# Optimization experiments

Hardware: AMD Instinct MI355X
Metric: run time of the kernel (lower is better)

Reference implementation:

```python
import jax, jax.numpy as jnp
import numpy as np

D_MODEL = 2048
N_HEADS = 16
D_K = D_MODEL // N_HEADS  # 128


def setup_inputs() -> dict:
    key = jax.random.key(0)
    ks = jax.random.split(key, 12)
    B, S = 2, 2048
    std = 1.0 / np.sqrt(D_MODEL)
    inp = {
        "query": jax.random.normal(ks[0], (B, S, D_MODEL), jnp.float32),
        "key": jax.random.normal(ks[1], (B, S, D_MODEL), jnp.float32),
        "value": jax.random.normal(ks[2], (B, S, D_MODEL), jnp.float32),
        "w_q": jax.random.normal(ks[3], (D_MODEL, D_MODEL), jnp.float32) * std,
        "b_q": jnp.zeros((D_MODEL,), jnp.float32),
        "w_k": jax.random.normal(ks[4], (D_MODEL, D_MODEL), jnp.float32) * std,
        "b_k": jnp.zeros((D_MODEL,), jnp.float32),
        "w_v": jax.random.normal(ks[5], (D_MODEL, D_MODEL), jnp.float32) * std,
        "b_v": jnp.zeros((D_MODEL,), jnp.float32),
        "w_o": jax.random.normal(ks[6], (D_MODEL, D_MODEL), jnp.float32) * std,
        "b_o": jnp.zeros((D_MODEL,), jnp.float32),
        # fractional scale numerator / denominator per head; ratio ~ 1/sqrt(d_k)
        "scale_alpha": jnp.full((N_HEADS,), 1.0, jnp.float32),
        "scale_beta": jnp.full((N_HEADS,), float(np.sqrt(D_K)), jnp.float32),
    }
    return inp


def reference(query, key, value, w_q, b_q, w_k, b_k, w_v, b_v, w_o, b_o,
              scale_alpha, scale_beta):
    B, S, _ = query.shape
    # projections (torch Linear: x @ W^T + b)
    Q = (query @ w_q.T + b_q).reshape(B, S, N_HEADS, D_K).transpose(0, 2, 1, 3)
    K = (key @ w_k.T + b_k).reshape(B, S, N_HEADS, D_K).transpose(0, 2, 1, 3)
    V = (value @ w_v.T + b_v).reshape(B, S, N_HEADS, D_K).transpose(0, 2, 1, 3)
    # per-head fractional scale alpha/beta (computed under no_grad in torch)
    scales = jax.lax.stop_gradient(scale_alpha / jnp.maximum(scale_beta, 1.0))
    scores = jnp.einsum("bhqd,bhkd->bhqk", Q, K) * scales[None, :, None, None]
    attn = jax.nn.softmax(scores, axis=-1)  # dropout is identity in eval
    out = jnp.einsum("bhqk,bhkd->bhqd", attn, V)
    out = out.transpose(0, 2, 1, 3).reshape(B, S, D_MODEL)
    return out @ w_o.T + b_o
```

## Files before the change

### kernel.cpp

```cpp
#include <hip/hip_runtime.h>
#include <cstdint>

#define S_LEN   2048
#define DMODEL  2048
#define NHEADS  16
#define DK      128
#define MROWS   4096

typedef _Float16 f16;
using f16x8 = __attribute__((ext_vector_type(8))) _Float16;
using f16x4 = __attribute__((ext_vector_type(4))) _Float16;
using f32x4 = __attribute__((ext_vector_type(4))) float;

typedef const __attribute__((address_space(1))) unsigned int gu32;
typedef __attribute__((address_space(3))) unsigned int lu32;

__device__ __forceinline__ void gl2lds16(const void* g, void* l) {
    __builtin_amdgcn_global_load_lds((gu32*)g, (lu32*)l, 16, 0, 0);
}

__global__ __launch_bounds__(256) void cvt_all(
    const float* __restrict__ q, const float* __restrict__ k,
    const float* __restrict__ v, const float* __restrict__ wq,
    const float* __restrict__ wk, const float* __restrict__ wv,
    const float* __restrict__ wo,
    f16* cq, f16* ck, f16* cv, f16* cwq, f16* cwk, f16* cwv, f16* cwo)
{
    const int b = blockIdx.x;
    const float* src; f16* dst; int base;
    if      (b <  2048) { src = q;  dst = cq;  base = b; }
    else if (b <  4096) { src = k;  dst = ck;  base = b - 2048; }
    else if (b <  6144) { src = v;  dst = cv;  base = b - 4096; }
    else if (b <  7168) { src = wq; dst = cwq; base = b - 6144; }
    else if (b <  8192) { src = wk; dst = cwk; base = b - 7168; }
    else if (b <  9216) { src = wv; dst = cwv; base = b - 8192; }
    else                { src = wo; dst = cwo; base = b - 9216; }
    const int i = base * 1024 + threadIdx.x;
#pragma unroll
    for (int u = 0; u < 4; ++u) {
        float4 x = ((const float4*)src)[i + u * 256];
        f16x4 o; o[0] = (f16)x.x; o[1] = (f16)x.y; o[2] = (f16)x.z; o[3] = (f16)x.w;
        ((f16x4*)dst)[i + u * 256] = o;
    }
}

template<int MODE>
__device__ __forceinline__ void gemm_core(
    const f16* __restrict__ A, const f16* __restrict__ W,
    const float* __restrict__ bias, void* __restrict__ Cout,
    const float* __restrict__ sa, const float* __restrict__ sb,
    f16* __restrict__ As, f16* __restrict__ Bs)
{
    const int tid = threadIdx.x;
    const int bm = blockIdx.y * 128;
    const int bn = blockIdx.x * 128;
    const int wid = tid >> 6;
    const int ln = tid & 15;
    const int quad = (tid & 63) >> 4;
    const int wm = (wid >> 1) * 64;
    const int wn = (wid & 1) * 64;
    const int K = DMODEL, N = DMODEL;

    f32x4 acc[4][4];
#pragma unroll
    for (int i = 0; i < 4; ++i)
#pragma unroll
        for (int j = 0; j < 4; ++j)
            acc[i][j] = (f32x4){0.f, 0.f, 0.f, 0.f};

    const int srow = tid >> 3;
    const int schk = ((tid & 7) ^ ((tid >> 3) & 7)) * 8;
    const f16* ga = A + (size_t)(bm + srow) * K + schk;
    const f16* gb = W + (size_t)(bn + srow) * K + schk;

    for (int k0 = 0; k0 < K; k0 += 64) {
        __syncthreads();
#pragma unroll
        for (int u = 0; u < 4; ++u)
            gl2lds16(ga + k0 + (size_t)(u * 32) * K, As + u * 2048 + tid * 8);
#pragma unroll
        for (int u = 0; u < 4; ++u)
            gl2lds16(gb + k0 + (size_t)(u * 32) * K, Bs + u * 2048 + tid * 8);
        __syncthreads();

#pragma unroll
        for (int kq = 0; kq < 2; ++kq) {
            f16x8 af[4], bf[4];
            const int rc = ((kq * 4 + quad) ^ (ln & 7)) * 8;
#pragma unroll
            for (int i = 0; i < 4; ++i)
                af[i] = *(const f16x8*)&As[(wm + i * 16 + ln) * 64 + rc];
#pragma unroll
            for (int j = 0; j < 4; ++j)
                bf[j] = *(const f16x8*)&Bs[(wn + j * 16 + ln) * 64 + rc];
#pragma unroll
            for (int i = 0; i < 4; ++i)
#pragma unroll
                for (int j = 0; j < 4; ++j)
                    acc[i][j] = __builtin_amdgcn_mfma_f32_16x16x32_f16(
                        af[i], bf[j], acc[i][j], 0, 0, 0);
        }
    }

#pragma unroll
    for (int j = 0; j < 4; ++j) {
        const int n = bn + wn + j * 16 + ln;
        const float bn_ = bias[n];
        const int h = n >> 7;
        const int d = n & (DK - 1);
        float scq = 1.0f;
        if constexpr (MODE == 3) scq = sa[h] / fmaxf(sb[h], 1.0f);
#pragma unroll
        for (int i = 0; i < 4; ++i) {
            const int m0 = bm + wm + i * 16 + quad * 4;
            if constexpr (MODE == 0) {
#pragma unroll
                for (int reg = 0; reg < 4; ++reg)
                    ((float*)Cout)[(size_t)(m0 + reg) * N + n] =
                        acc[i][j][reg] + bn_;
            } else if constexpr (MODE == 2) {
                const int bb = m0 >> 11;
                const int ss = m0 & (S_LEN - 1);
                f16x4 o;
#pragma unroll
                for (int reg = 0; reg < 4; ++reg)
                    o[reg] = (f16)(acc[i][j][reg] + bn_);
                *(f16x4*)&((f16*)Cout)[
                    (((size_t)(bb * NHEADS + h) * DK + d) * S_LEN + ss)] = o;
            } else {
                const int bb = m0 >> 11;
                const int ss = m0 & (S_LEN - 1);
                f16* dst = (f16*)Cout +
                    (((size_t)(bb * NHEADS + h) * S_LEN + ss) * DK + d);
#pragma unroll
                for (int reg = 0; reg < 4; ++reg) {
                    float v = acc[i][j][reg] + bn_;
                    if constexpr (MODE == 3) v *= scq;
                    dst[reg * DK] = (f16)v;
                }
            }
        }
    }
}

__global__ __launch_bounds__(256) void qkv_gemm(
    const f16* Aq, const f16* Ak, const f16* Av,
    const f16* Wq, const f16* Wk, const f16* Wv,
    const float* bq, const float* bk, const float* bv,
    f16* Oq, f16* Ok, f16* Ov, const float* sa, const float* sb)
{
    __shared__ f16 As[128 * 64];
    __shared__ f16 Bs[128 * 64];
    const int z = blockIdx.z;
    if (z == 0)      gemm_core<3>(Aq, Wq, bq, (void*)Oq, sa, sb, As, Bs);
    else if (z == 1) gemm_core<1>(Ak, Wk, bk, (void*)Ok, nullptr, nullptr, As, Bs);
    else             gemm_core<2>(Av, Wv, bv, (void*)Ov, nullptr, nullptr, As, Bs);
}

__global__ __launch_bounds__(256) void out_gemm(
    const f16* A, const f16* W, const float* bias, float* O)
{
    __shared__ f16 As[128 * 64];
    __shared__ f16 Bs[128 * 64];
    gemm_core<0>(A, W, bias, (void*)O, nullptr, nullptr, As, Bs);
}

__global__ __launch_bounds__(256, 2) void flash_v6(
    const f16* __restrict__ Qg, const f16* __restrict__ Kg,
    const f16* __restrict__ VTg, f16* __restrict__ AO)
{
    __shared__ f16 Ks[2][4 * 64 * 32];
    __shared__ f16 Vs[2 * 128 * 32];
    __shared__ f16 Ps[2 * 128 * 32];
    __shared__ float l_buf[2 * 128];

    const int tid = threadIdx.x;
    const int wid = tid >> 6;
    const int ln = tid & 15;
    const int quad = (tid & 63) >> 4;
    const int wq = wid & 1;
    const int wc = wid >> 1;

    const int lin = blockIdx.x + (blockIdx.y << 4);
    const int swz = (lin & 7) * 64 + (lin >> 3);
    const int q0 = (swz & 15) * 128;
    const int bh = swz >> 4;

    const int koff = (quad ^ ((ln >> 1) & 3)) * 8;
    const int soff_sw = ((tid & 3) ^ ((tid >> 3) & 3)) * 8;

    f16x8 qf[4][4];
    const f16* Qbase = Qg + ((size_t)bh * S_LEN + q0 + wq * 64) * DK;
#pragma unroll
    for (int nt = 0; nt < 4; ++nt)
#pragma unroll
        for (int kc = 0; kc < 4; ++kc)
            qf[nt][kc] = *(const f16x8*)(Qbase + (size_t)(nt * 16 + ln) * DK
                                         + kc * 32 + quad * 8);

    f32x4 o[4][4];
    float lp[4] = {0.f, 0.f, 0.f, 0.f};
#pragma unroll
    for (int i = 0; i < 4; ++i)
#pragma unroll
        for (int j = 0; j < 4; ++j)
            o[i][j] = (f32x4){0.f, 0.f, 0.f, 0.f};

    const f16* Kgb = Kg + (size_t)bh * S_LEN * DK;
    const f16* Vgb = VTg + (size_t)bh * DK * S_LEN;
    const int srow = tid >> 2;

#pragma unroll
    for (int j = 0; j < 4; ++j)
        gl2lds16(Kgb + (size_t)(srow)*DK + j * 32 + soff_sw,
                 &Ks[0][j * 2048 + tid * 8]);

    for (int kt = 0; kt < S_LEN / 64; ++kt) {
        asm volatile("s_waitcnt lgkmcnt(0)" ::: "memory");
        __builtin_amdgcn_s_barrier();
        __builtin_amdgcn_sched_barrier(0);

#pragma unroll
        for (int j = 0; j < 4; ++j)
            gl2lds16(Vgb + (size_t)(srow + (j & 1) * 64) * S_LEN
                         + kt * 64 + (j >> 1) * 32 + soff_sw,
                     Vs + (j >> 1) * 4096 + (j & 1) * 2048 + tid * 8);

        asm volatile("s_waitcnt vmcnt(4)" ::: "memory");
        __builtin_amdgcn_s_barrier();
        __builtin_amdgcn_sched_barrier(0);

        const f16* Kb = &Ks[kt & 1][0];
        f32x4 s[2][4];
#pragma unroll
        for (int mt = 0; mt < 2; ++mt)
#pragma unroll
            for (int nt = 0; nt < 4; ++nt)
                s[mt][nt] = (f32x4){0.f, 0.f, 0.f, 0.f};
        __builtin_amdgcn_s_setprio(1);
#pragma unroll
        for (int kc = 0; kc < 4; ++kc) {
            f16x8 kf0 = *(const f16x8*)&Kb[kc * 2048 + (wc * 32 + ln) * 32 + koff];
            f16x8 kf1 = *(const f16x8*)&Kb[kc * 2048 + (wc * 32 + 16 + ln) * 32 + koff];
#pragma unroll
            for (int nt = 0; nt < 4; ++nt) {
                s[0][nt] = __builtin_amdgcn_mfma_f32_16x16x32_f16(kf0, qf[nt][kc], s[0][nt], 0, 0, 0);
                s[1][nt] = __builtin_amdgcn_mfma_f32_16x16x32_f16(kf1, qf[nt][kc], s[1][nt], 0, 0, 0);
            }
        }
        __builtin_amdgcn_s_setprio(0);

        if (kt + 1 < S_LEN / 64) {
#pragma unroll
            for (int j = 0; j < 4; ++j)
                gl2lds16(Kgb + (size_t)((kt + 1) * 64 + srow) * DK + j * 32 + soff_sw,
                         &Ks[(kt + 1) & 1][j * 2048 + tid * 8]);
        }

#pragma unroll
        for (int mt = 0; mt < 2; ++mt) {
#pragma unroll
            for (int nt = 0; nt < 4; ++nt) {
                const float p0 = __expf(s[mt][nt][0]);
                const float p1 = __expf(s[mt][nt][1]);
                const float p2 = __expf(s[mt][nt][2]);
                const float p3 = __expf(s[mt][nt][3]);
                lp[nt] += (p0 + p1) + (p2 + p3);
                f16x4 pk;
                pk[0] = (f16)p0; pk[1] = (f16)p1; pk[2] = (f16)p2; pk[3] = (f16)p3;
                const int pchunk = ((mt * 2 + (quad >> 1)) ^ ((ln >> 1) & 3)) * 8
                                   + (quad & 1) * 4;
                *(f16x4*)&Ps[wc * 4096 + (wq * 64 + nt * 16 + ln) * 32 + pchunk] = pk;
            }
        }

        if (kt + 1 < S_LEN / 64) asm volatile("s_waitcnt vmcnt(4)" ::: "memory");
        else                     asm volatile("s_waitcnt vmcnt(0)" ::: "memory");
        asm volatile("s_waitcnt lgkmcnt(0)" ::: "memory");
        __builtin_amdgcn_s_barrier();
        __builtin_amdgcn_sched_barrier(0);

        __builtin_amdgcn_s_setprio(1);
#pragma unroll
        for (int cc = 0; cc < 2; ++cc) {
            f16x8 pf[4];
#pragma unroll
            for (int mtq = 0; mtq < 4; ++mtq)
                pf[mtq] = *(const f16x8*)&Ps[cc * 4096 + (wq * 64 + mtq * 16 + ln) * 32 + koff];
#pragma unroll
            for (int ntd = 0; ntd < 4; ++ntd) {
                f16x8 vf = *(const f16x8*)&Vs[cc * 4096 + (wc * 64 + ntd * 16 + ln) * 32 + koff];
#pragma unroll
                for (int mtq = 0; mtq < 4; ++mtq)
                    o[mtq][ntd] = __builtin_amdgcn_mfma_f32_16x16x32_f16(
                        pf[mtq], vf, o[mtq][ntd], 0, 0, 0);
            }
        }
        __builtin_amdgcn_s_setprio(0);
    }

#pragma unroll
    for (int nt = 0; nt < 4; ++nt) {
        float v = lp[nt];
        v += __shfl_xor(v, 16, 64);
        v += __shfl_xor(v, 32, 64);
        lp[nt] = v;
    }
    __syncthreads();
    if (quad == 0) {
#pragma unroll
        for (int nt = 0; nt < 4; ++nt)
            l_buf[wc * 128 + wq * 64 + nt * 16 + ln] = lp[nt];
    }
    __syncthreads();

    const int b = bh >> 4;
    const int h = bh & (NHEADS - 1);
#pragma unroll
    for (int mtq = 0; mtq < 4; ++mtq) {
#pragma unroll
        for (int reg = 0; reg < 4; ++reg) {
            const int ql = wq * 64 + mtq * 16 + quad * 4 + reg;
            const float inv = 1.0f / (l_buf[ql] + l_buf[128 + ql]);
            f16* dst = AO + ((size_t)b * S_LEN + q0 + ql) * DMODEL + h * DK + wc * 64;
#pragma unroll
            for (int ntd = 0; ntd < 4; ++ntd)
                dst[ntd * 16 + ln] = (f16)(o[mtq][ntd][reg] * inv);
        }
    }
}

extern "C" void kernel_launch(void* const* d_in, const int* in_sizes, int n_in,
                              void* d_out, int out_size, void* d_ws, size_t ws_size,
                              hipStream_t stream)
{
    (void)in_sizes; (void)n_in; (void)out_size; (void)ws_size;
    const float* query = (const float*)d_in[0];
    const float* key_  = (const float*)d_in[1];
    const float* value = (const float*)d_in[2];
    const float* w_q = (const float*)d_in[3];
    const float* b_q = (const float*)d_in[4];
    const float* w_k = (const float*)d_in[5];
    const float* b_k = (const float*)d_in[6];
    const float* w_v = (const float*)d_in[7];
    const float* b_v = (const float*)d_in[8];
    const float* w_o = (const float*)d_in[9];
    const float* b_o = (const float*)d_in[10];
    const float* s_alpha = (const float*)d_in[11];
    const float* s_beta  = (const float*)d_in[12];
    float* out = (float*)d_out;

    const size_t T = (size_t)MROWS * DMODEL;
    const size_t Wn = (size_t)DMODEL * DMODEL;
    f16* base = (f16*)d_ws;
    f16* c_q = base;
    f16* c_k = base + T;
    f16* c_v = base + 2 * T;
    f16* Qh  = base + 3 * T;
    f16* wq16 = base + 4 * T;
    f16* wk16 = wq16 + Wn;
    f16* wv16 = wk16 + Wn;
    f16* wo16 = wv16 + Wn;
    f16* Kh  = (f16*)d_out;
    f16* VT  = Kh + T;
    f16* AOh = c_v;

    cvt_all<<<dim3(10240), dim3(256), 0, stream>>>(
        query, key_, value, w_q, w_k, w_v, w_o,
        c_q, c_k, c_v, wq16, wk16, wv16, wo16);

    dim3 qkv_grid(DMODEL / 128, MROWS / 128, 3);
    qkv_gemm<<<qkv_grid, dim3(256), 0, stream>>>(c_q, c_k, c_v, wq16, wk16, wv16,
                                                 b_q, b_k, b_v, Qh, Kh, VT,
                                                 s_alpha, s_beta);

    dim3 flash_grid(S_LEN / 128, 2 * NHEADS);
    flash_v6<<<flash_grid, dim3(256), 0, stream>>>(Qh, Kh, VT, AOh);

    dim3 out_grid(DMODEL / 128, MROWS / 128);
    out_gemm<<<out_grid, dim3(256), 0, stream>>>(AOh, wo16, b_o, out);
}
```

Measured before the change: 451.8 us.

## Single-buffer K tile in LDS with register-staged prefetch in flash kernel

The double-buffered K tile in LDS is replaced by one buffer. The next K tile is prefetched into registers with ordinary global loads and written to LDS after the post-softmax barrier, while the P·V MFMAs run. One barrier per iteration is dropped and the launch-bounds occupancy hint of 2 is removed. LDS use drops, but register pressure rises, and the full vmcnt(0) wait now blocks on both V and the K prefetch before P·V.

```diff
diff --git a/kernel.cpp b/kernel.cpp
--- a/kernel.cpp
+++ b/kernel.cpp
@@ -165,11 +165,11 @@
     gemm_core<0>(A, W, bias, (void*)O, nullptr, nullptr, As, Bs);
 }
 
-__global__ __launch_bounds__(256, 2) void flash_v6(
+__global__ __launch_bounds__(256) void flash_v7(
     const f16* __restrict__ Qg, const f16* __restrict__ Kg,
     const f16* __restrict__ VTg, f16* __restrict__ AO)
 {
-    __shared__ f16 Ks[2][4 * 64 * 32];
+    __shared__ f16 Ks[4 * 64 * 32];
     __shared__ f16 Vs[2 * 128 * 32];
     __shared__ f16 Ps[2 * 128 * 32];
     __shared__ float l_buf[2 * 128];
@@ -212,25 +212,33 @@
 
 #pragma unroll
     for (int j = 0; j < 4; ++j)
-        gl2lds16(Kgb + (size_t)(srow)*DK + j * 32 + soff_sw,
-                 &Ks[0][j * 2048 + tid * 8]);
-
-    for (int kt = 0; kt < S_LEN / 64; ++kt) {
+        gl2lds16(Kgb + (size_t)srow * DK + j * 32 + soff_sw,
+                 &Ks[j * 2048 + tid * 8]);
+    asm volatile("s_waitcnt vmcnt(0)" ::: "memory");
+    __builtin_amdgcn_s_barrier();
+    __builtin_amdgcn_sched_barrier(0);
+
+    constexpr int NT = S_LEN / 64;
+    for (int kt = 0; kt < NT; ++kt) {
         asm volatile("s_waitcnt lgkmcnt(0)" ::: "memory");
         __builtin_amdgcn_s_barrier();
         __builtin_amdgcn_sched_barrier(0);
 
+        const bool nl = (kt + 1 < NT);
+
+        f16x8 kpre[4];
+        if (nl) {
+#pragma unroll
+            for (int j = 0; j < 4; ++j)
+                kpre[j] = *(const f16x8*)(Kgb
+                    + (size_t)((kt + 1) * 64 + srow) * DK + j * 32 + soff_sw);
+        }
 #pragma unroll
         for (int j = 0; j < 4; ++j)
             gl2lds16(Vgb + (size_t)(srow + (j & 1) * 64) * S_LEN
                          + kt * 64 + (j >> 1) * 32 + soff_sw,
                      Vs + (j >> 1) * 4096 + (j & 1) * 2048 + tid * 8);
 
-        asm volatile("s_waitcnt vmcnt(4)" ::: "memory");
-        __builtin_amdgcn_s_barrier();
-        __builtin_amdgcn_sched_barrier(0);
-
-        const f16* Kb = &Ks[kt & 1][0];
         f32x4 s[2][4];
 #pragma unroll
         for (int mt = 0; mt < 2; ++mt)
@@ -240,8 +248,8 @@
         __builtin_amdgcn_s_setprio(1);
 #pragma unroll
         for (int kc = 0; kc < 4; ++kc) {
-            f16x8 kf0 = *(const f16x8*)&Kb[kc * 2048 + (wc * 32 + ln) * 32 + koff];
-            f16x8 kf1 = *(const f16x8*)&Kb[kc * 2048 + (wc * 32 + 16 + ln) * 32 + koff];
+            f16x8 kf0 = *(const f16x8*)&Ks[kc * 2048 + (wc * 32 + ln) * 32 + koff];
+            f16x8 kf1 = *(const f16x8*)&Ks[kc * 2048 + (wc * 32 + 16 + ln) * 32 + koff];
 #pragma unroll
             for (int nt = 0; nt < 4; ++nt) {
                 s[0][nt] = __builtin_amdgcn_mfma_f32_16x16x32_f16(kf0, qf[nt][kc], s[0][nt], 0, 0, 0);
@@ -249,13 +257,6 @@
             }
         }
         __builtin_amdgcn_s_setprio(0);
-
-        if (kt + 1 < S_LEN / 64) {
-#pragma unroll
-            for (int j = 0; j < 4; ++j)
-                gl2lds16(Kgb + (size_t)((kt + 1) * 64 + srow) * DK + j * 32 + soff_sw,
-                         &Ks[(kt + 1) & 1][j * 2048 + tid * 8]);
-        }
 
 #pragma unroll
         for (int mt = 0; mt < 2; ++mt) {
@@ -274,11 +275,16 @@
             }
         }
 
-        if (kt + 1 < S_LEN / 64) asm volatile("s_waitcnt vmcnt(4)" ::: "memory");
-        else                     asm volatile("s_waitcnt vmcnt(0)" ::: "memory");
+        asm volatile("s_waitcnt vmcnt(0)" ::: "memory");
         asm volatile("s_waitcnt lgkmcnt(0)" ::: "memory");
         __builtin_amdgcn_s_barrier();
         __builtin_amdgcn_sched_barrier(0);
+
+        if (nl) {
+#pragma unroll
+            for (int j = 0; j < 4; ++j)
+                *(f16x8*)&Ks[j * 2048 + tid * 8] = kpre[j];
+        }
 
         __builtin_amdgcn_s_setprio(1);
 #pragma unroll
@@ -375,7 +381,7 @@
                                                  s_alpha, s_beta);
 
     dim3 flash_grid(S_LEN / 128, 2 * NHEADS);
-    flash_v6<<<flash_grid, dim3(256), 0, stream>>>(Qh, Kh, VT, AOh);
+    flash_v7<<<flash_grid, dim3(256), 0, stream>>>(Qh, Kh, VT, AOh);
 
     dim3 out_grid(DMODEL / 128, MROWS / 128);
     out_gemm<<<out_grid, dim3(256), 0, stream>>>(AOh, wo16, b_o, out);
```

Measured after the change: 486.7 us. +7.7%, slower.
